# Optimization experiments

Measured on AMD Instinct MI355X. Metric: run time of the kernel, lower is better.

The kernel has to match this reference:

```python
import jax, jax.numpy as jnp
import numpy as np

S = 1024   # speakers_per_batch
U = 64     # utterances_per_speaker
E = 256    # model_embedding_size


def setup_inputs() -> dict:
    key = jax.random.key(0)
    k1, _ = jax.random.split(key)
    # embeds as produced by forward(): relu'd then L2-normalized rows
    raw = jax.nn.relu(jax.random.normal(k1, (S * U, E), dtype=jnp.float32))
    embeds = raw / (jnp.linalg.norm(raw, axis=1, keepdims=True) + 1e-12)
    return {
        "embeds": embeds,
        "similarity_weight": jnp.array([10.0], dtype=jnp.float32),
        "similarity_bias": jnp.array([-5.0], dtype=jnp.float32),
    }


def reference(embeds, similarity_weight, similarity_bias):
    e = embeds.reshape(S, U, E)                      # [S,U,E]
    # inclusive centroids (per speaker)
    c_incl = jnp.mean(e, axis=1)                     # [S,E]
    incl_norm = jnp.linalg.norm(c_incl, axis=1)      # [S]
    # exclusive centroids (leave-one-out per utterance)
    c_excl = (jnp.sum(e, axis=1, keepdims=True) - e) / (U - 1)  # [S,U,E]
    excl_norm = jnp.linalg.norm(c_excl, axis=2)      # [S,U]
    # off-diagonal (k != j): cosine vs inclusive centroid of speaker k
    sim = jnp.einsum('jue,ke->juk', e, c_incl) / incl_norm       # [S,U,S]
    # diagonal (k == j): cosine vs own exclusive centroid
    diag = jnp.einsum('jue,jue->ju', e, c_excl) / excl_norm      # [S,U]
    idx = jnp.arange(S)
    sim = sim.at[idx, :, idx].set(diag)
    sim = sim * similarity_weight[0] + similarity_bias[0]
    # cross-entropy against ground truth speaker ids
    logits = sim.reshape(S * U, S)                   # [SU,S]
    gt = jnp.repeat(jnp.arange(S), U)                # [SU]
    logp = jax.nn.log_softmax(logits, axis=-1)
    loss = -jnp.mean(jnp.take_along_axis(logp, gt[:, None], axis=1))
    preds = jnp.argmax(logits, axis=1)
    accuracy = jnp.mean((preds == gt).astype(jnp.float32))
    return loss, accuracy
```

## Files before the change

kernel.cpp:

```cpp
#include <hip/hip_runtime.h>
#include <math.h>

#define NS 1024
#define NU 64
#define NE 256

typedef __attribute__((ext_vector_type(4))) float f32x4;

__device__ static inline unsigned int pk4_fp8(float a, float b, float c,
                                              float d) {
  int r = 0;
  r = __builtin_amdgcn_cvt_pk_fp8_f32(a, b, r, false);
  r = __builtin_amdgcn_cvt_pk_fp8_f32(c, d, r, true);
  return (unsigned int)r;
}


__global__ __launch_bounds__(256) void centroid_kernel(
    const float* __restrict__ embeds, unsigned int* __restrict__ Cb,
    unsigned long long* __restrict__ Ab, float* __restrict__ normsum,
    float* __restrict__ ssumG, unsigned int* __restrict__ pmaxG,
    float* __restrict__ out) {
  int k = blockIdx.x;
  int t = threadIdx.x;
  if (t < 64) {
    ssumG[k * 64 + t] = 0.f;
    pmaxG[k * 64 + t] = 0u;
  }
  int wave = t >> 6, e4 = t & 63;

  const float4* base =
      (const float4*)(embeds + (size_t)k * NU * NE) + wave * 16 * 64 + e4;
  float4 s = {0.f, 0.f, 0.f, 0.f};
#pragma unroll
  for (int i = 0; i < 16; ++i) {
    float4 v = base[i * 64];
    s.x += v.x; s.y += v.y; s.z += v.z; s.w += v.w;
  }
  __shared__ float4 ps[4][64];
  ps[wave][e4] = s;
  __syncthreads();
  if (t < 64) {
    float4 a = ps[0][t], b = ps[1][t], c = ps[2][t], d = ps[3][t];
    float4 s4;
    s4.x = a.x + b.x + c.x + d.x;
    s4.y = a.y + b.y + c.y + d.y;
    s4.z = a.z + b.z + c.z + d.z;
    s4.w = a.w + b.w + c.w + d.w;
    float sq = s4.x * s4.x + s4.y * s4.y + s4.z * s4.z + s4.w * s4.w;
#pragma unroll
    for (int off = 32; off; off >>= 1) sq += __shfl_xor(sq, off, 64);
    float nrm = sqrtf(sq);
    float inv = 1.f / nrm;
    unsigned int v = pk4_fp8(s4.x * inv, s4.y * inv, s4.z * inv, s4.w * inv);
    int idx = (k >> 4) * 1024 + (t >> 3) * 128 +
              ((((t >> 1) & 3) * 16 + (k & 15)) << 1) + (t & 1);
    Cb[idx] = v;
    if (t == 0) {
      normsum[k] = nrm;
      if (k == 0) { out[0] = 0.f; out[1] = 0.f; }
    }
  }

  {
    int tile = t >> 6;
    int l = t & 63;
    int m = l & 15, qq = l >> 4;
    const float* rowp = embeds + (size_t)(k * 64 + tile * 16 + m) * NE;
    size_t basei = ((size_t)k * 4 + tile) * 512 + l;
#pragma unroll
    for (int sI = 0; sI < 8; ++sI) {
      int k0 = sI * 32 + qq * 8;
      float4 x = *(const float4*)(rowp + k0);
      float4 y = *(const float4*)(rowp + k0 + 4);
      unsigned int lo = pk4_fp8(x.x, x.y, x.z, x.w);
      unsigned int hi = pk4_fp8(y.x, y.y, y.z, y.w);
      Ab[basei + sI * 64] = ((unsigned long long)hi << 32) | lo;
    }
  }
}

__global__ __launch_bounds__(256, 2) void main_kernel(
    const long* __restrict__ Ab, const long* __restrict__ Cb,
    const float* __restrict__ normsum, const float* __restrict__ wp,
    const float* __restrict__ bp, float* __restrict__ ssumG,
    unsigned int* __restrict__ pmaxG, float* __restrict__ pdiagG) {
  int t = threadIdx.x;
  int wave = t >> 6, lane = t & 63;
  int c = lane & 15, q = lane >> 4;
  int b = blockIdx.x;
  int rg = b >> 1;
  int h = b & 1;
  int jspk = rg * 2 + (wave >> 1);
  int r0 = rg * 128 + wave * 32;

  float w = *wp, bia = *bp;
  const float L2E = 1.4426950408889634f;
  float M0 = fabsf(w) + bia;
  float wl = w * L2E;
  float cl = (bia - M0) * L2E;
  float ns = normsum[jspk];

  int fb = h * 32 * 512 + lane;

  long bfA[4], bfB[4];
#pragma unroll
  for (int s = 0; s < 4; ++s) bfA[s] = Cb[fb + s * 64];
#pragma unroll
  for (int s = 0; s < 4; ++s) bfB[s] = Cb[fb + (4 + s) * 64];

  long af[2][8];
#pragma unroll
  for (int mt = 0; mt < 2; ++mt) {
    int ab = ((r0 >> 4) + mt) * 512 + lane;
#pragma unroll
    for (int s = 0; s < 8; ++s) af[mt][s] = Ab[ab + s * 64];
  }

  float ssum[2][4];
  float pm[2][4];
#pragma unroll
  for (int mt = 0; mt < 2; ++mt)
#pragma unroll
    for (int r = 0; r < 4; ++r) {
      ssum[mt][r] = 0.f;
      pm[mt][r] = 0.f;
    }

#pragma unroll 1
  for (int T = 0; T < 32; ++T) {
    f32x4 acc[2];
    acc[0] = (f32x4){0.f, 0.f, 0.f, 0.f};
    acc[1] = (f32x4){0.f, 0.f, 0.f, 0.f};
    int nb = fb + (T + 1) * 512;
    bool more = (T + 1 < 32);
#pragma unroll
    for (int s = 0; s < 4; ++s) {
      acc[0] = __builtin_amdgcn_mfma_f32_16x16x32_fp8_fp8(af[0][s], bfA[s],
                                                          acc[0], 0, 0, 0);
      acc[1] = __builtin_amdgcn_mfma_f32_16x16x32_fp8_fp8(af[1][s], bfA[s],
                                                          acc[1], 0, 0, 0);
    }
    if (more) {
#pragma unroll
      for (int s = 0; s < 4; ++s) bfA[s] = Cb[nb + s * 64];
    }
#pragma unroll
    for (int s = 0; s < 4; ++s) {
      acc[0] = __builtin_amdgcn_mfma_f32_16x16x32_fp8_fp8(af[0][4 + s], bfB[s],
                                                          acc[0], 0, 0, 0);
      acc[1] = __builtin_amdgcn_mfma_f32_16x16x32_fp8_fp8(af[1][4 + s], bfB[s],
                                                          acc[1], 0, 0, 0);
    }
    if (more) {
#pragma unroll
      for (int s = 0; s < 4; ++s) bfB[s] = Cb[nb + (4 + s) * 64];
    }

    int gt = h * 32 + T;
    bool diagstep = ((jspk >> 4) == gt);
#pragma unroll
    for (int mt = 0; mt < 2; ++mt) {
      f32x4 a = acc[mt];
      if (diagstep && c == (jspk & 15)) {
#pragma unroll
        for (int r = 0; r < 4; ++r) {
          float Sv = a[r] * ns;
          float den = fmaxf(fmaf(ns, ns, 1.f) - 2.f * Sv, 1e-30f);
          float val = (Sv - 1.f) * __frsqrt_rn(den);
          float pd = exp2f(fmaf(val, wl, cl));
          pdiagG[r0 + mt * 16 + q * 4 + r] = pd;
          a[r] = val;
        }
      }
#pragma unroll
      for (int r = 0; r < 4; ++r) {
        float p = exp2f(fmaf(a[r], wl, cl));
        ssum[mt][r] += p;
        pm[mt][r] = fmaxf(pm[mt][r], p);
      }
    }
  }

#pragma unroll
  for (int mt = 0; mt < 2; ++mt)
#pragma unroll
    for (int r = 0; r < 4; ++r) {
      float s = ssum[mt][r];
      s += __shfl_xor(s, 1, 64);
      s += __shfl_xor(s, 2, 64);
      s += __shfl_xor(s, 4, 64);
      s += __shfl_xor(s, 8, 64);
      float m = pm[mt][r];
      m = fmaxf(m, __shfl_xor(m, 1, 64));
      m = fmaxf(m, __shfl_xor(m, 2, 64));
      m = fmaxf(m, __shfl_xor(m, 4, 64));
      m = fmaxf(m, __shfl_xor(m, 8, 64));
      if (c == 0) {
        int row = r0 + mt * 16 + q * 4 + r;
        atomicAdd(&ssumG[row], s);
        atomicMax(&pmaxG[row], __float_as_uint(m));
      }
    }
}

__global__ __launch_bounds__(256) void reduce_kernel(
    const float* __restrict__ ssumG, const unsigned int* __restrict__ pmaxG,
    const float* __restrict__ pdiagG, float* __restrict__ out) {
  int i = blockIdx.x * 256 + threadIdx.x;
  float pd = pdiagG[i];
  float lossr = __logf(ssumG[i] / pd);
  float corr = (pd >= __uint_as_float(pmaxG[i])) ? 1.f : 0.f;
#pragma unroll
  for (int off = 32; off; off >>= 1) {
    lossr += __shfl_xor(lossr, off, 64);
    corr += __shfl_xor(corr, off, 64);
  }
  __shared__ float pl[4], pc[4];
  int wave = threadIdx.x >> 6, lane = threadIdx.x & 63;
  if (lane == 0) { pl[wave] = lossr; pc[wave] = corr; }
  __syncthreads();
  if (threadIdx.x == 0) {
    const float inv = 1.f / (float)(NS * NU);
    atomicAdd(&out[0], (pl[0] + pl[1] + pl[2] + pl[3]) * inv);
    atomicAdd(&out[1], (pc[0] + pc[1] + pc[2] + pc[3]) * inv);
  }
}

extern "C" void kernel_launch(void* const* d_in, const int* in_sizes, int n_in,
                              void* d_out, int out_size, void* d_ws,
                              size_t ws_size, hipStream_t stream) {
  const float* embeds = (const float*)d_in[0];
  const float* w = (const float*)d_in[1];
  const float* b = (const float*)d_in[2];
  float* out = (float*)d_out;
  char* ws = (char*)d_ws;
  unsigned int* Cb = (unsigned int*)ws;
  unsigned int* pmaxG = (unsigned int*)(ws + (256 << 10));
  float* ssumG = (float*)(ws + (512 << 10));
  float* pdiagG = (float*)(ws + (768 << 10));
  float* normsum = (float*)(ws + (1024 << 10));
  unsigned long long* Ab =
      (unsigned long long*)(ws + (1056 << 10));

  centroid_kernel<<<NS, 256, 0, stream>>>(embeds, Cb, Ab, normsum, ssumG,
                                          pmaxG, out);
  main_kernel<<<1024, 256, 0, stream>>>((const long*)Ab, (const long*)Cb,
                                        normsum, w, b, ssumG, pmaxG, pdiagG);
  reduce_kernel<<<NS * NU / 256, 256, 0, stream>>>(ssumG, pmaxG, pdiagG, out);
}
```

Baseline: 150.5 us.

## Software-pipeline MFMA tiles with epilogue, widen loads to 128-bit, raise occupancy

Reorders the fp8 packed A and C buffers so each lane can fetch two 64-bit MFMA operands with one 128-bit load. Restructures the main loop into a two-stage ping-pong, so each tile's MFMAs run while the previous tile's exp/sum/max epilogue executes. MFMA issue priority is raised with s_setprio. Launch bounds go from 2 to 4 blocks per CU, which limits registers per thread and may cause spills with the doubled accumulators and buffers.

New measurement: 145.1 us. -3.6%, faster.

```diff
diff --git a/kernel.cpp b/kernel.cpp
--- a/kernel.cpp
+++ b/kernel.cpp
@@ -6,6 +6,7 @@
 #define NE 256
 
 typedef __attribute__((ext_vector_type(4))) float f32x4;
+typedef long i64x2 __attribute__((ext_vector_type(2)));
 
 __device__ static inline unsigned int pk4_fp8(float a, float b, float c,
                                               float d) {
@@ -53,8 +54,9 @@
     float nrm = sqrtf(sq);
     float inv = 1.f / nrm;
     unsigned int v = pk4_fp8(s4.x * inv, s4.y * inv, s4.z * inv, s4.w * inv);
-    int idx = (k >> 4) * 1024 + (t >> 3) * 128 +
-              ((((t >> 1) & 3) * 16 + (k & 15)) << 1) + (t & 1);
+    int lane_ = (((t >> 1) & 3) * 16 + (k & 15));
+    int idx = (k >> 4) * 1024 + (t >> 4) * 256 + lane_ * 4 +
+              (((t >> 3) & 1) << 1) + (t & 1);
     Cb[idx] = v;
     if (t == 0) {
       normsum[k] = nrm;
@@ -67,20 +69,30 @@
     int l = t & 63;
     int m = l & 15, qq = l >> 4;
     const float* rowp = embeds + (size_t)(k * 64 + tile * 16 + m) * NE;
-    size_t basei = ((size_t)k * 4 + tile) * 512 + l;
-#pragma unroll
-    for (int sI = 0; sI < 8; ++sI) {
-      int k0 = sI * 32 + qq * 8;
-      float4 x = *(const float4*)(rowp + k0);
-      float4 y = *(const float4*)(rowp + k0 + 4);
-      unsigned int lo = pk4_fp8(x.x, x.y, x.z, x.w);
-      unsigned int hi = pk4_fp8(y.x, y.y, y.z, y.w);
-      Ab[basei + sI * 64] = ((unsigned long long)hi << 32) | lo;
-    }
-  }
-}
-
-__global__ __launch_bounds__(256, 2) void main_kernel(
+    i64x2* Ab2 = (i64x2*)Ab;
+    size_t base2 = ((size_t)k * 4 + tile) * 256 + l;
+#pragma unroll
+    for (int s2 = 0; s2 < 4; ++s2) {
+      unsigned long long u[2];
+#pragma unroll
+      for (int half = 0; half < 2; ++half) {
+        int sI = 2 * s2 + half;
+        int k0 = sI * 32 + qq * 8;
+        float4 x = *(const float4*)(rowp + k0);
+        float4 y = *(const float4*)(rowp + k0 + 4);
+        unsigned int lo = pk4_fp8(x.x, x.y, x.z, x.w);
+        unsigned int hi = pk4_fp8(y.x, y.y, y.z, y.w);
+        u[half] = ((unsigned long long)hi << 32) | lo;
+      }
+      i64x2 v;
+      v.x = (long)u[0];
+      v.y = (long)u[1];
+      Ab2[base2 + s2 * 64] = v;
+    }
+  }
+}
+
+__global__ __launch_bounds__(256, 4) void main_kernel(
     const long* __restrict__ Ab, const long* __restrict__ Cb,
     const float* __restrict__ normsum, const float* __restrict__ wp,
     const float* __restrict__ bp, float* __restrict__ ssumG,
@@ -101,20 +113,19 @@
   float cl = (bia - M0) * L2E;
   float ns = normsum[jspk];
 
-  int fb = h * 32 * 512 + lane;
-
-  long bfA[4], bfB[4];
-#pragma unroll
-  for (int s = 0; s < 4; ++s) bfA[s] = Cb[fb + s * 64];
-#pragma unroll
-  for (int s = 0; s < 4; ++s) bfB[s] = Cb[fb + (4 + s) * 64];
+  const i64x2* Av = (const i64x2*)Ab;
+  const i64x2* Bv = (const i64x2*)Cb;
 
   long af[2][8];
 #pragma unroll
   for (int mt = 0; mt < 2; ++mt) {
-    int ab = ((r0 >> 4) + mt) * 512 + lane;
-#pragma unroll
-    for (int s = 0; s < 8; ++s) af[mt][s] = Ab[ab + s * 64];
+    int ab2 = ((r0 >> 4) + mt) * 256 + lane;
+#pragma unroll
+    for (int s2 = 0; s2 < 4; ++s2) {
+      i64x2 v = Av[ab2 + s2 * 64];
+      af[mt][2 * s2] = v.x;
+      af[mt][2 * s2 + 1] = v.y;
+    }
   }
 
   float ssum[2][4];
@@ -127,41 +138,36 @@
       pm[mt][r] = 0.f;
     }
 
-#pragma unroll 1
-  for (int T = 0; T < 32; ++T) {
-    f32x4 acc[2];
-    acc[0] = (f32x4){0.f, 0.f, 0.f, 0.f};
-    acc[1] = (f32x4){0.f, 0.f, 0.f, 0.f};
-    int nb = fb + (T + 1) * 512;
-    bool more = (T + 1 < 32);
-#pragma unroll
-    for (int s = 0; s < 4; ++s) {
-      acc[0] = __builtin_amdgcn_mfma_f32_16x16x32_fp8_fp8(af[0][s], bfA[s],
-                                                          acc[0], 0, 0, 0);
-      acc[1] = __builtin_amdgcn_mfma_f32_16x16x32_fp8_fp8(af[1][s], bfA[s],
-                                                          acc[1], 0, 0, 0);
-    }
-    if (more) {
-#pragma unroll
-      for (int s = 0; s < 4; ++s) bfA[s] = Cb[nb + s * 64];
-    }
-#pragma unroll
-    for (int s = 0; s < 4; ++s) {
-      acc[0] = __builtin_amdgcn_mfma_f32_16x16x32_fp8_fp8(af[0][4 + s], bfB[s],
-                                                          acc[0], 0, 0, 0);
-      acc[1] = __builtin_amdgcn_mfma_f32_16x16x32_fp8_fp8(af[1][4 + s], bfB[s],
-                                                          acc[1], 0, 0, 0);
-    }
-    if (more) {
-#pragma unroll
-      for (int s = 0; s < 4; ++s) bfB[s] = Cb[nb + (4 + s) * 64];
-    }
-
-    int gt = h * 32 + T;
+  auto prefetch = [&](i64x2 (&BF)[4], int Tt) {
+    int cb = (h * 32 + Tt) * 256 + lane;
+#pragma unroll
+    for (int s2 = 0; s2 < 4; ++s2) BF[s2] = Bv[cb + s2 * 64];
+  };
+
+  auto tile = [&](f32x4 (&ACC)[2], const i64x2 (&BF)[4]) {
+    ACC[0] = (f32x4){0.f, 0.f, 0.f, 0.f};
+    ACC[1] = (f32x4){0.f, 0.f, 0.f, 0.f};
+    __builtin_amdgcn_s_setprio(1);
+#pragma unroll
+    for (int s2 = 0; s2 < 4; ++s2) {
+      ACC[0] = __builtin_amdgcn_mfma_f32_16x16x32_fp8_fp8(af[0][2 * s2],
+                                                          BF[s2].x, ACC[0], 0, 0, 0);
+      ACC[1] = __builtin_amdgcn_mfma_f32_16x16x32_fp8_fp8(af[1][2 * s2],
+                                                          BF[s2].x, ACC[1], 0, 0, 0);
+      ACC[0] = __builtin_amdgcn_mfma_f32_16x16x32_fp8_fp8(af[0][2 * s2 + 1],
+                                                          BF[s2].y, ACC[0], 0, 0, 0);
+      ACC[1] = __builtin_amdgcn_mfma_f32_16x16x32_fp8_fp8(af[1][2 * s2 + 1],
+                                                          BF[s2].y, ACC[1], 0, 0, 0);
+    }
+    __builtin_amdgcn_s_setprio(0);
+  };
+
+  auto epilogue = [&](f32x4 (&ACC)[2], int Tt) {
+    int gt = h * 32 + Tt;
     bool diagstep = ((jspk >> 4) == gt);
 #pragma unroll
     for (int mt = 0; mt < 2; ++mt) {
-      f32x4 a = acc[mt];
+      f32x4 a = ACC[mt];
       if (diagstep && c == (jspk & 15)) {
 #pragma unroll
         for (int r = 0; r < 4; ++r) {
@@ -180,7 +186,25 @@
         pm[mt][r] = fmaxf(pm[mt][r], p);
       }
     }
-  }
+  };
+
+  i64x2 bf0[4], bf1[4];
+  f32x4 accA[2], accB[2];
+  prefetch(bf0, 0);
+  prefetch(bf1, 1);
+  tile(accA, bf0);
+#pragma unroll 1
+  for (int T = 1; T < 31; T += 2) {
+    prefetch(bf0, T + 1);
+    tile(accB, bf1);
+    epilogue(accA, T - 1);
+    prefetch(bf1, T + 2);
+    tile(accA, bf0);
+    epilogue(accB, T);
+  }
+  tile(accB, bf1);
+  epilogue(accA, 30);
+  epilogue(accB, 31);
 
 #pragma unroll
   for (int mt = 0; mt < 2; ++mt)
```
